# Performance work log

Measured on AMD Instinct MI355X. Metric: run time of the kernel, lower is better.

Reference implementation:

```python
import jax, jax.numpy as jnp
import numpy as np

N_GRAPHS = 64   # number of graphs in the batch
H = 128         # hidden dim
L = 3           # num_conv_layers
OUT = 64        # out_feature


def setup_inputs() -> dict:
    key = jax.random.key(0)
    ks = jax.random.split(key, 12)
    N, E, R, C = 10000, 160000, 2, 2
    s = 1.0 / np.sqrt(H)
    inp = {
        'x': jax.random.normal(ks[0], (N, H), jnp.float32),
        'edge_attr': jax.random.normal(ks[1], (E, H), jnp.float32),
        'node_mask': jax.random.uniform(ks[2], (R, C, N, 1), jnp.float32),
        'bond_W': jax.random.normal(ks[3], (L, H, H), jnp.float32) * s,
        'bond_b': jnp.zeros((L, H), jnp.float32),
        'eps': jnp.zeros((L,), jnp.float32),
        'conv_W1': jax.random.normal(ks[4], (L, H, H), jnp.float32) * s,
        'conv_b1': jnp.zeros((L, H), jnp.float32),
        'conv_W2': jax.random.normal(ks[5], (L, H, H), jnp.float32) * s,
        'conv_b2': jnp.zeros((L, H), jnp.float32),
        'mlp_W1': jax.random.normal(ks[6], (H, H), jnp.float32) * s,
        'mlp_b1': jnp.zeros((H,), jnp.float32),
        'mlp_W2': jax.random.normal(ks[7], (H, OUT), jnp.float32) * s,
        'mlp_b2': jnp.zeros((OUT,), jnp.float32),
        'edge_index': jax.random.randint(ks[8], (2, E), 0, N),
        'batch': jnp.sort(jax.random.randint(ks[9], (N,), 0, N_GRAPHS)),
    }
    return inp


def reference(x, edge_attr, node_mask, bond_W, bond_b, eps,
              conv_W1, conv_b1, conv_W2, conv_b2,
              mlp_W1, mlp_b1, mlp_W2, mlp_b2,
              edge_index, batch):
    gelu = lambda v: jax.nn.gelu(v, approximate=False)  # torch exact gelu
    R, C, N, _ = node_mask.shape
    src, dst = edge_index[0], edge_index[1]
    # edge_mask[r,c,e] = node_mask[r,c,src[e]] * node_mask[r,c,dst[e]]
    edge_mask = node_mask[:, :, src, :] * node_mask[:, :, dst, :]  # [R,C,E,1]
    # replica-offset graph ids: [R*C*N]
    batch_full = jnp.tile(batch, R * C) + jnp.repeat(jnp.arange(R * C), N) * N_GRAPHS
    # x repeated over (R, C): [R,C,N,H]
    h = jnp.broadcast_to(x[None, None], (R, C, N, x.shape[-1]))
    for i in range(L):
        emb = edge_attr @ bond_W[i] + bond_b[i]                    # [E,H]
        msg = gelu(h[:, :, src, :] + emb[None, None]) * edge_mask  # [R,C,E,H]
        agg = jnp.zeros_like(h).at[:, :, dst, :].add(msg)          # scatter_sum
        out = (1.0 + eps[i]) * h + agg
        out = gelu(out @ conv_W1[i] + conv_b1[i]) @ conv_W2[i] + conv_b2[i]
        h = gelu(out)  # norm=Identity, dropout=0
    hf = h.reshape(-1, h.shape[-1])                               # [R*C*N,H]
    y = gelu(hf @ mlp_W1 + mlp_b1) @ mlp_W2 + mlp_b2              # [R*C*N,OUT]
    fm = node_mask.reshape(-1, 1)
    D = R * N_GRAPHS * C
    num = jax.ops.segment_sum(y * fm, batch_full, num_segments=D)
    den = jax.ops.segment_sum(fm, batch_full, num_segments=D)
    return num / jnp.maximum(den, 1e-12)
```

## Files before the change

### kernel.cpp

```cpp
#include <hip/hip_runtime.h>

constexpr int H    = 128;
constexpr int NN   = 10000;
constexpr int EE   = 160000;
constexpr int RCN  = 4;
constexpr int NG   = 64;
constexpr int OUTF = 64;
constexpr int DSEG = 256;

using short8 = __attribute__((ext_vector_type(8))) short;
using f32x4  = __attribute__((ext_vector_type(4))) float;

__device__ __forceinline__ float gelu_f(float x){
  float z  = x*0.70710678118654752440f;
  float az = fabsf(z);
  float t  = __builtin_amdgcn_rcpf(fmaf(az, 0.3275911f, 1.0f));
  float e  = __expf(-z*z);
  float poly = fmaf(fmaf(fmaf(fmaf(1.061405429f, t, -1.453152027f),
                              t, 1.421413741f),
                         t, -0.284496736f),
                    t, 0.254829592f) * t;
  float er = fmaf(-poly, e, 1.0f);
  er = copysignf(er, z);
  return 0.5f*x*(1.0f + er);
}

__device__ __forceinline__ void split2(float x, unsigned short& h, unsigned short& m){
  unsigned int u = __float_as_uint(x);
  unsigned int rh = u + 0x7FFF + ((u>>16)&1);
  h = (unsigned short)(rh>>16);
  float fh = __uint_as_float((unsigned int)h << 16);
  float r1 = x - fh;
  unsigned int u1 = __float_as_uint(r1);
  unsigned int rm = u1 + 0x7FFF + ((u1>>16)&1);
  m = (unsigned short)(rm>>16);
}

__device__ __forceinline__ unsigned short bf16rne(float x){
  unsigned int u = __float_as_uint(x);
  return (unsigned short)((u + 0x7FFF + ((u>>16)&1))>>16);
}
__device__ __forceinline__ float bf2f(unsigned short v){
  return __uint_as_float((unsigned int)v << 16);
}

__global__ void k_hist(const int* __restrict__ dst, int* __restrict__ cnt){
  int e = blockIdx.x*256 + threadIdx.x;
  if(e < EE) atomicAdd(&cnt[dst[e]], 1);
}

__global__ __launch_bounds__(1024) void k_scan(const int* __restrict__ cnt,
                                               int* __restrict__ rs, int* __restrict__ cur){
  __shared__ int part[1024];
  int t = threadIdx.x;
  const int CH = 10;
  int base = t*CH;
  int s = 0;
  #pragma unroll
  for(int j=0;j<CH;j++){ int i = base+j; if(i<NN) s += cnt[i]; }
  part[t] = s;
  __syncthreads();
  for(int off=1; off<1024; off<<=1){
    int v = (t>=off) ? part[t-off] : 0;
    __syncthreads();
    part[t] += v;
    __syncthreads();
  }
  int run = (t==0) ? 0 : part[t-1];
  #pragma unroll
  for(int j=0;j<CH;j++){
    int i = base+j;
    if(i<NN){ rs[i] = run; cur[i] = run; run += cnt[i]; }
  }
  if(t == 1023) rs[NN] = part[1023];
}

__global__ void k_fill(const int* __restrict__ dst,
                       int* __restrict__ cur, int* __restrict__ eid){
  int e = blockIdx.x*256 + threadIdx.x;
  if(e >= EE) return;
  int p = atomicAdd(&cur[dst[e]], 1);
  eid[p] = e;
}

__global__ __launch_bounds__(256) void k_sortcsr(const int* __restrict__ rs, int* __restrict__ eid,
                          const int* __restrict__ src, int* __restrict__ esrc){
  int wid  = (blockIdx.x*256 + threadIdx.x) >> 6;
  int lane = threadIdx.x & 63;
  if(wid >= NN) return;
  int jb = rs[wid], je = rs[wid+1];
  int deg = je - jb;
  if(deg <= 0) return;
  if(deg == 1){
    if(lane == 0) esrc[jb] = src[eid[jb]];
    return;
  }
  if(deg <= 64){
    int v = (lane < deg) ? eid[jb + lane] : 0x7FFFFFFF;
    #pragma unroll
    for(int k=2; k<=64; k<<=1){
      #pragma unroll
      for(int j=k>>1; j>0; j>>=1){
        int o = __shfl_xor(v, j, 64);
        bool desc  = (lane & k) != 0;
        bool lower = (lane & j) == 0;
        v = ((lower != desc) ? min(v,o) : max(v,o));
      }
    }
    if(lane < deg){
      eid[jb+lane]  = v;
      esrc[jb+lane] = src[v];
    }
  } else if(lane == 0){
    for(int j=jb+1; j<je; j++){
      int v = eid[j];
      int k = j-1;
      while(k >= jb && eid[k] > v){ eid[k+1] = eid[k]; k--; }
      eid[k+1] = v;
    }
    for(int j=jb; j<je; j++) esrc[j] = src[eid[j]];
  }
}

__global__ void k_gbounds(const int* __restrict__ batch, int* __restrict__ gs){
  int g = threadIdx.x;
  if(g > NG) return;
  if(g == NG){ gs[NG] = NN; return; }
  int lo = 0, hi = NN;
  while(lo < hi){
    int mid = (lo+hi)>>1;
    if(batch[mid] < g) lo = mid+1; else hi = mid;
  }
  gs[g] = lo;
}

__global__ void k_emaskp(const int* __restrict__ src, const int* __restrict__ dst,
                         const int* __restrict__ eid, const float* __restrict__ nm,
                         float4* __restrict__ em4p){
  int j = blockIdx.x*256 + threadIdx.x;
  if(j >= EE) return;
  int e = eid[j];
  int s = src[e], d = dst[e];
  float4 m;
  m.x = nm[0*NN+s]*nm[0*NN+d];
  m.y = nm[1*NN+s]*nm[1*NN+d];
  m.z = nm[2*NN+s]*nm[2*NN+d];
  m.w = nm[3*NN+s]*nm[3*NN+d];
  em4p[j] = m;
}

__global__ void k_splitW(const float* __restrict__ W, unsigned short* __restrict__ oh,
                         unsigned short* __restrict__ om, int nmat, int N){
  int tid = blockIdx.x*256 + threadIdx.x;
  int total = nmat*128*N;
  if(tid >= total) return;
  int mat = tid / (128*N);
  int rem = tid - mat*(128*N);
  int k = rem / N;
  int n = rem - k*N;
  int NF = N >> 4;
  int ks = k >> 5, kk = k & 31;
  int nf = n >> 4;
  int lane = (n & 15) + 16*((kk & 15) >> 2);
  int e = 4*(kk >> 4) + (kk & 3);
  size_t idx = (size_t)mat*128*N + ((size_t)(ks*NF + nf)*64 + lane)*8 + e;
  unsigned short hh, mm;
  split2(W[tid], hh, mm);
  oh[idx] = hh; om[idx] = mm;
}

__global__ void k_splitA(const float* __restrict__ A, const int* __restrict__ eid,
                         unsigned short* __restrict__ oh){
  int tid = blockIdx.x*256 + threadIdx.x;
  if(tid >= EE*32) return;
  int j = tid >> 5, kq = tid & 31;
  int k = kq*4;
  int rsrc = eid[j];
  float4 v = *(const float4*)&A[(size_t)rsrc*H + k];
  ushort4 hh;
  hh.x = bf16rne(v.x); hh.y = bf16rne(v.y);
  hh.z = bf16rne(v.z); hh.w = bf16rne(v.w);
  *(ushort4*)&oh[(size_t)j*H + k] = hh;
}

template<int NFO, bool A2, bool GELU, int OMODE>
__global__ __launch_bounds__(256) void k_sgemm(
    const unsigned short* __restrict__ Ah, const unsigned short* __restrict__ Am,
    const unsigned short* __restrict__ Wh, const unsigned short* __restrict__ Wm,
    const float* __restrict__ bias, float* __restrict__ Cf,
    unsigned short* __restrict__ Oh, unsigned short* __restrict__ Om, int nrows){
  int t = threadIdx.x;
  int w = t >> 6, lane = t & 63;
  int m15 = lane & 15, kg = lane >> 4;
  int rowbase = blockIdx.x*128;

  const int SMAX = 4*NFO - 1;
  auto ldW = [&](int s, short8* d){
    size_t widx = ((size_t)s*64 + lane)*8;
    d[0] = *(const short8*)&Wh[widx];
    d[1] = *(const short8*)&Wm[widx];
  };

  int arow[2];
  #pragma unroll
  for(int mf=0;mf<2;mf++){
    int r = rowbase + w*32 + mf*16 + m15;
    arow[mf] = (r < nrows) ? r : (nrows-1);
  }

  f32x4 acc[2][NFO];
  #pragma unroll
  for(int mf=0;mf<2;mf++)
    #pragma unroll
    for(int nf=0;nf<NFO;nf++) acc[mf][nf] = (f32x4){0.f,0.f,0.f,0.f};

  short8 cw[2], nw[2];
  ldW(0, cw);
  ldW(1 <= SMAX ? 1 : SMAX, nw);

  for(int ks=0;ks<4;ks++){
    short8 ah[2], am[2];
    #pragma unroll
    for(int mf=0;mf<2;mf++){
      size_t base = (size_t)arow[mf]*H + ks*32 + kg*4;
      ushort4 hlo = *(const ushort4*)&Ah[base];
      ushort4 hhi = *(const ushort4*)&Ah[base + 16];
      ah[mf] = (short8){(short)hlo.x,(short)hlo.y,(short)hlo.z,(short)hlo.w,
                        (short)hhi.x,(short)hhi.y,(short)hhi.z,(short)hhi.w};
      if(A2){
        ushort4 mlo = *(const ushort4*)&Am[base];
        ushort4 mhi = *(const ushort4*)&Am[base + 16];
        am[mf] = (short8){(short)mlo.x,(short)mlo.y,(short)mlo.z,(short)mlo.w,
                          (short)mhi.x,(short)mhi.y,(short)mhi.z,(short)mhi.w};
      }
    }
    #pragma unroll
    for(int nf=0;nf<NFO;nf++){
      int s = ks*NFO + nf;
      short8 pw[2];
      ldW(s+2 <= SMAX ? s+2 : SMAX, pw);
      #pragma unroll
      for(int mf=0;mf<2;mf++){
        acc[mf][nf] = __builtin_amdgcn_mfma_f32_16x16x32_bf16(ah[mf], cw[0], acc[mf][nf], 0,0,0);
        acc[mf][nf] = __builtin_amdgcn_mfma_f32_16x16x32_bf16(ah[mf], cw[1], acc[mf][nf], 0,0,0);
        if(A2)
          acc[mf][nf] = __builtin_amdgcn_mfma_f32_16x16x32_bf16(am[mf], cw[0], acc[mf][nf], 0,0,0);
      }
      cw[0]=nw[0]; cw[1]=nw[1];
      nw[0]=pw[0]; nw[1]=pw[1];
    }
  }
  #pragma unroll
  for(int mf=0;mf<2;mf++){
    #pragma unroll
    for(int nf=0;nf<NFO;nf++){
      int gcol = nf*16 + m15;
      float bv = bias[gcol];
      #pragma unroll
      for(int r=0;r<4;r++){
        int grow = rowbase + w*32 + mf*16 + kg*4 + r;
        if(grow >= nrows) continue;
        float v = acc[mf][nf][r] + bv;
        if(GELU) v = gelu_f(v);
        size_t idx = (size_t)grow*(NFO*16) + gcol;
        if(OMODE == 0) Cf[idx] = v;
        if(OMODE == 1){
          unsigned short hh, mm2;
          split2(v, hh, mm2);
          Oh[idx] = hh; Om[idx] = mm2;
        }
        if(OMODE == 2) Oh[idx] = bf16rne(v);
      }
    }
  }
}

template<bool FIRST>
__global__ __launch_bounds__(256) void k_agg(const float* __restrict__ hin,
                       const unsigned short* __restrict__ embB, const float4* __restrict__ em4p,
                       const int* __restrict__ rs, const int* __restrict__ esrc,
                       const float* __restrict__ epsp,
                       unsigned short* __restrict__ Th, unsigned short* __restrict__ Tm){
  int t = threadIdx.x;
  int w = t >> 6;
  int lane = t & 63;
  int half = lane >> 5;
  int l32 = lane & 31;
  int n = blockIdx.x*4 + w;
  int d0 = l32*4;
  int rc0 = half*2, rc1 = rc0+1;
  float4 acc0 = {0.f,0.f,0.f,0.f}, acc1 = {0.f,0.f,0.f,0.f};
  int jb = rs[n], je = rs[n+1];

  float4 evs[3], h0s[3], h1s[3];
  float  m0s[3], m1s[3];

  auto ld = [&](int j, int slot){
    int s = esrc[j];
    ushort4 e4 = *(const ushort4*)&embB[(size_t)j*H + d0];
    evs[slot].x = bf2f(e4.x); evs[slot].y = bf2f(e4.y);
    evs[slot].z = bf2f(e4.z); evs[slot].w = bf2f(e4.w);
    float4 m = em4p[j];
    m0s[slot] = half ? m.z : m.x;
    m1s[slot] = half ? m.w : m.y;
    if(FIRST){
      h0s[slot] = *(const float4*)&hin[(size_t)s*H + d0];
      h1s[slot] = h0s[slot];
    } else {
      h0s[slot] = *(const float4*)&hin[((size_t)s*RCN + rc0)*H + d0];
      h1s[slot] = *(const float4*)&hin[((size_t)s*RCN + rc1)*H + d0];
    }
  };

  if(jb < je){
    ld(jb, 0);
    if(jb+1 < je) ld(jb+1, 1);
    if(jb+2 < je) ld(jb+2, 2);
    for(int j=jb; j<je; j++){
      float4 ev0 = evs[0], h00 = h0s[0], h10 = h1s[0];
      float  m00 = m0s[0], m10 = m1s[0];
      evs[0]=evs[1]; h0s[0]=h0s[1]; h1s[0]=h1s[1]; m0s[0]=m0s[1]; m1s[0]=m1s[1];
      evs[1]=evs[2]; h0s[1]=h0s[2]; h1s[1]=h1s[2]; m0s[1]=m0s[2]; m1s[1]=m1s[2];
      if(j+3 < je) ld(j+3, 2);
      if(FIRST){
        float gx = gelu_f(h00.x+ev0.x);
        float gy = gelu_f(h00.y+ev0.y);
        float gz = gelu_f(h00.z+ev0.z);
        float gw = gelu_f(h00.w+ev0.w);
        acc0.x += gx*m00; acc0.y += gy*m00; acc0.z += gz*m00; acc0.w += gw*m00;
        acc1.x += gx*m10; acc1.y += gy*m10; acc1.z += gz*m10; acc1.w += gw*m10;
      } else {
        acc0.x += gelu_f(h00.x+ev0.x)*m00;
        acc0.y += gelu_f(h00.y+ev0.y)*m00;
        acc0.z += gelu_f(h00.z+ev0.z)*m00;
        acc0.w += gelu_f(h00.w+ev0.w)*m00;
        acc1.x += gelu_f(h10.x+ev0.x)*m10;
        acc1.y += gelu_f(h10.y+ev0.y)*m10;
        acc1.z += gelu_f(h10.z+ev0.z)*m10;
        acc1.w += gelu_f(h10.w+ev0.w)*m10;
      }
    }
  }
  float e1 = 1.0f + epsp[0];
  #pragma unroll
  for(int p=0;p<2;p++){
    int rc = p ? rc1 : rc0;
    float4 ac = p ? acc1 : acc0;
    const float* hb = FIRST ? (hin + (size_t)n*H) : (hin + ((size_t)n*RCN + rc)*H);
    float4 hv = *(const float4*)&hb[d0];
    float4 o;
    o.x = e1*hv.x + ac.x; o.y = e1*hv.y + ac.y;
    o.z = e1*hv.z + ac.z; o.w = e1*hv.w + ac.w;
    int row = n*RCN + rc;
    ushort4 hh, mm;
    split2(o.x, hh.x, mm.x);
    split2(o.y, hh.y, mm.y);
    split2(o.z, hh.z, mm.z);
    split2(o.w, hh.w, mm.w);
    size_t idx = (size_t)row*H + d0;
    *(ushort4*)&Th[idx] = hh;
    *(ushort4*)&Tm[idx] = mm;
  }
}

__global__ __launch_bounds__(64) void k_pool(const float* __restrict__ y, const float* __restrict__ nm,
                       const int* __restrict__ gs, float* __restrict__ out){
  int seg = blockIdx.x;
  int rc = seg / NG;
  int g  = seg - rc*NG;
  int c  = threadIdx.x;
  int nb = gs[g], ne = gs[g+1];
  float num = 0.f, den = 0.f;
  for(int n=nb; n<ne; n++){
    float w = nm[rc*NN + n];
    num += y[((size_t)n*RCN + rc)*OUTF + c] * w;
    den += w;
  }
  out[seg*OUTF + c] = num / fmaxf(den, 1e-12f);
}

extern "C" void kernel_launch(void* const* d_in, const int* in_sizes, int n_in,
                              void* d_out, int out_size, void* d_ws, size_t ws_size,
                              hipStream_t stream){
  const float* x         = (const float*)d_in[0];
  const float* edge_attr = (const float*)d_in[1];
  const float* node_mask = (const float*)d_in[2];
  const float* bond_W    = (const float*)d_in[3];
  const float* bond_b    = (const float*)d_in[4];
  const float* epsv      = (const float*)d_in[5];
  const float* conv_W1   = (const float*)d_in[6];
  const float* conv_b1   = (const float*)d_in[7];
  const float* conv_W2   = (const float*)d_in[8];
  const float* conv_b2   = (const float*)d_in[9];
  const float* mlp_W1    = (const float*)d_in[10];
  const float* mlp_b1    = (const float*)d_in[11];
  const float* mlp_W2    = (const float*)d_in[12];
  const float* mlp_b2    = (const float*)d_in[13];
  const int*   eidx      = (const int*)d_in[14];
  const int*   batch     = (const int*)d_in[15];
  const int* srcp = eidx;
  const int* dstp = eidx + EE;

  char* p = (char*)d_ws;
  auto alloc = [&](size_t bytes)->char*{
    char* r = p; p += (bytes + 255) & ~size_t(255); return r;
  };
  float*  h    = (float*) alloc((size_t)RCN*NN*H*4);
  unsigned short* embB = (unsigned short*)alloc((size_t)EE*H*2);
  float4* em4p = (float4*)alloc((size_t)EE*16);
  float*  y    = (float*) alloc((size_t)RCN*NN*OUTF*4);
  int*    cnt  = (int*)   alloc((size_t)NN*4);
  int*    rs   = (int*)   alloc((size_t)(NN+1)*4);
  int*    cur  = (int*)   alloc((size_t)NN*4);
  int*    eid  = (int*)   alloc((size_t)EE*4);
  int*    esrc = (int*)   alloc((size_t)EE*4);
  int*    gs   = (int*)   alloc((size_t)(NG+1)*4);
  unsigned short* WBh  = (unsigned short*)alloc((size_t)3*16384*2);
  unsigned short* WBm  = (unsigned short*)alloc((size_t)3*16384*2);
  unsigned short* WC1h = (unsigned short*)alloc((size_t)3*16384*2);
  unsigned short* WC1m = (unsigned short*)alloc((size_t)3*16384*2);
  unsigned short* WC2h = (unsigned short*)alloc((size_t)3*16384*2);
  unsigned short* WC2m = (unsigned short*)alloc((size_t)3*16384*2);
  unsigned short* WM1h = (unsigned short*)alloc((size_t)16384*2);
  unsigned short* WM1m = (unsigned short*)alloc((size_t)16384*2);
  unsigned short* WM2h = (unsigned short*)alloc((size_t)8192*2);
  unsigned short* WM2m = (unsigned short*)alloc((size_t)8192*2);
  unsigned short* EAh  = (unsigned short*)alloc((size_t)EE*H*2);
  const size_t NPB = (size_t)RCN*NN*H*2;
  unsigned short* TBh = (unsigned short*)alloc(NPB);
  unsigned short* TBm = (unsigned short*)alloc(NPB);
  unsigned short* Uh  = (unsigned short*)alloc(NPB);
  unsigned short* Um  = (unsigned short*)alloc(NPB);
  if((size_t)(p - (char*)d_ws) > ws_size) return;

  hipMemsetAsync(cnt, 0, (size_t)NN*4, stream);

  k_hist    <<<(EE+255)/256, 256, 0, stream>>>(dstp, cnt);
  k_scan    <<<1, 1024, 0, stream>>>(cnt, rs, cur);
  k_fill    <<<(EE+255)/256, 256, 0, stream>>>(dstp, cur, eid);
  k_sortcsr <<<(NN*64+255)/256, 256, 0, stream>>>(rs, eid, srcp, esrc);
  k_emaskp  <<<(EE+255)/256, 256, 0, stream>>>(srcp, dstp, eid, node_mask, em4p);
  k_splitA  <<<EE*32/256, 256, 0, stream>>>(edge_attr, eid, EAh);
  k_gbounds <<<1, 128, 0, stream>>>(batch, gs);
  k_splitW  <<<192, 256, 0, stream>>>(bond_W,  WBh,  WBm,  3, 128);
  k_splitW  <<<192, 256, 0, stream>>>(conv_W1, WC1h, WC1m, 3, 128);
  k_splitW  <<<192, 256, 0, stream>>>(conv_W2, WC2h, WC2m, 3, 128);
  k_splitW  <<<64,  256, 0, stream>>>(mlp_W1,  WM1h, WM1m, 1, 128);
  k_splitW  <<<32,  256, 0, stream>>>(mlp_W2,  WM2h, WM2m, 1, 64);

  const int NROWS = RCN*NN;
  const int GB_E = EE/128;
  const int GB_N = (NROWS+127)/128;
  for(int l=0; l<3; l++){
    size_t wo = (size_t)l*16384;
    k_sgemm<8,false,false,2><<<GB_E, 256, 0, stream>>>(
        EAh, nullptr, WBh+wo, WBm+wo, bond_b + l*H, nullptr, embB, nullptr, EE);
    if(l == 0)
      k_agg<true ><<<NN/4, 256, 0, stream>>>(x, embB, em4p, rs, esrc, epsv + l, TBh, TBm);
    else
      k_agg<false><<<NN/4, 256, 0, stream>>>(h, embB, em4p, rs, esrc, epsv + l, TBh, TBm);
    k_sgemm<8,true,true,1><<<GB_N, 256, 0, stream>>>(
        TBh, TBm, WC1h+wo, WC1m+wo, conv_b1 + l*H, nullptr, Uh, Um, NROWS);
    if(l < 2)
      k_sgemm<8,true,true,0><<<GB_N, 256, 0, stream>>>(
          Uh, Um, WC2h+wo, WC2m+wo, conv_b2 + l*H, h, nullptr, nullptr, NROWS);
    else
      k_sgemm<8,true,true,1><<<GB_N, 256, 0, stream>>>(
          Uh, Um, WC2h+wo, WC2m+wo, conv_b2 + l*H, nullptr, TBh, TBm, NROWS);
  }
  k_sgemm<8,true,true,1><<<GB_N, 256, 0, stream>>>(
      TBh, TBm, WM1h, WM1m, mlp_b1, nullptr, Uh, Um, NROWS);
  k_sgemm<4,true,false,0><<<GB_N, 256, 0, stream>>>(
      Uh, Um, WM2h, WM2m, mlp_b2, y, nullptr, nullptr, NROWS);
  k_pool<<<DSEG, 64, 0, stream>>>(y, node_mask, gs, (float*)d_out);
}
```

Measured before the change: 613.3 us.

## Fuse back-to-back GEMM pairs through LDS and rotate aggregation prefetch registers

Adds a k_fuse2 kernel that computes the first GEMM plus GELU, keeps the split bf16 hi/lo intermediate in shared memory per wave, and then runs the second GEMM from LDS. This replaces the two-kernel conv MLP and final MLP chains, removing the round trip of the intermediate U buffers through global memory and some launches. The aggregation loop is also reworked to rotate three named register slots instead of shifting arrays, avoiding register moves. In exchange, the 67KB LDS footprint per block limits occupancy. In the last layer the kernel also reads and writes TBh/TBm in place, which is only safe because each block reads its own rows before writing them.

```diff
diff --git a/kernel.cpp b/kernel.cpp
--- a/kernel.cpp
+++ b/kernel.cpp
@@ -275,6 +275,201 @@
   }
 }
 
+template<int NFO2, bool G2, int OMODE>
+__global__ __launch_bounds__(256) void k_fuse2(
+    const unsigned short* __restrict__ Ah, const unsigned short* __restrict__ Am,
+    const unsigned short* __restrict__ W1h, const unsigned short* __restrict__ W1m,
+    const float* __restrict__ b1,
+    const unsigned short* __restrict__ W2h, const unsigned short* __restrict__ W2m,
+    const float* __restrict__ b2,
+    float* __restrict__ Cf,
+    unsigned short* __restrict__ Oh, unsigned short* __restrict__ Om, int nrows){
+  __shared__ unsigned int Ul[4*32*132];
+  int t = threadIdx.x;
+  int w = t >> 6, lane = t & 63;
+  int m15 = lane & 15, kg = lane >> 4;
+  int rowbase = blockIdx.x*128;
+  unsigned int* Uw = &Ul[w*32*132];
+
+  int arow[2];
+  #pragma unroll
+  for(int mf=0;mf<2;mf++){
+    int r = rowbase + w*32 + mf*16 + m15;
+    arow[mf] = (r < nrows) ? r : (nrows-1);
+  }
+
+  {
+    const int SMAX = 31;
+    auto ldW = [&](int s, short8* d){
+      size_t widx = ((size_t)s*64 + lane)*8;
+      d[0] = *(const short8*)&W1h[widx];
+      d[1] = *(const short8*)&W1m[widx];
+    };
+    f32x4 acc[2][8];
+    #pragma unroll
+    for(int mf=0;mf<2;mf++)
+      #pragma unroll
+      for(int nf=0;nf<8;nf++) acc[mf][nf] = (f32x4){0.f,0.f,0.f,0.f};
+    short8 cw[2], nw[2];
+    ldW(0, cw); ldW(1, nw);
+    for(int ks=0;ks<4;ks++){
+      short8 ah[2], am[2];
+      #pragma unroll
+      for(int mf=0;mf<2;mf++){
+        size_t base = (size_t)arow[mf]*H + ks*32 + kg*4;
+        ushort4 hlo = *(const ushort4*)&Ah[base];
+        ushort4 hhi = *(const ushort4*)&Ah[base + 16];
+        ushort4 mlo = *(const ushort4*)&Am[base];
+        ushort4 mhi = *(const ushort4*)&Am[base + 16];
+        ah[mf] = (short8){(short)hlo.x,(short)hlo.y,(short)hlo.z,(short)hlo.w,
+                          (short)hhi.x,(short)hhi.y,(short)hhi.z,(short)hhi.w};
+        am[mf] = (short8){(short)mlo.x,(short)mlo.y,(short)mlo.z,(short)mlo.w,
+                          (short)mhi.x,(short)mhi.y,(short)mhi.z,(short)mhi.w};
+      }
+      #pragma unroll
+      for(int nf=0;nf<8;nf++){
+        int s = ks*8 + nf;
+        short8 pw[2];
+        ldW(s+2 <= SMAX ? s+2 : SMAX, pw);
+        #pragma unroll
+        for(int mf=0;mf<2;mf++){
+          acc[mf][nf] = __builtin_amdgcn_mfma_f32_16x16x32_bf16(ah[mf], cw[0], acc[mf][nf], 0,0,0);
+          acc[mf][nf] = __builtin_amdgcn_mfma_f32_16x16x32_bf16(ah[mf], cw[1], acc[mf][nf], 0,0,0);
+          acc[mf][nf] = __builtin_amdgcn_mfma_f32_16x16x32_bf16(am[mf], cw[0], acc[mf][nf], 0,0,0);
+        }
+        cw[0]=nw[0]; cw[1]=nw[1];
+        nw[0]=pw[0]; nw[1]=pw[1];
+      }
+    }
+    #pragma unroll
+    for(int mf=0;mf<2;mf++){
+      #pragma unroll
+      for(int nf=0;nf<8;nf++){
+        float bv = b1[nf*16 + m15];
+        #pragma unroll
+        for(int r=0;r<4;r++){
+          float v = gelu_f(acc[mf][nf][r] + bv);
+          unsigned short hh, mm2;
+          split2(v, hh, mm2);
+          int wrow = mf*16 + kg*4 + r;
+          Uw[wrow*132 + nf*16 + m15] = (unsigned)hh | ((unsigned)mm2 << 16);
+        }
+      }
+    }
+  }
+  __syncthreads();
+
+  {
+    const int SMAX = 4*NFO2 - 1;
+    auto ldW = [&](int s, short8* d){
+      size_t widx = ((size_t)s*64 + lane)*8;
+      d[0] = *(const short8*)&W2h[widx];
+      d[1] = *(const short8*)&W2m[widx];
+    };
+    f32x4 acc[2][NFO2];
+    #pragma unroll
+    for(int mf=0;mf<2;mf++)
+      #pragma unroll
+      for(int nf=0;nf<NFO2;nf++) acc[mf][nf] = (f32x4){0.f,0.f,0.f,0.f};
+    short8 cw[2], nw[2];
+    ldW(0, cw); ldW(1 <= SMAX ? 1 : SMAX, nw);
+    for(int ks=0;ks<4;ks++){
+      short8 ah[2], am[2];
+      #pragma unroll
+      for(int mf=0;mf<2;mf++){
+        const unsigned int* base = &Uw[(mf*16 + m15)*132 + ks*32 + kg*4];
+        uint4 q0 = *(const uint4*)base;
+        uint4 q1 = *(const uint4*)(base + 16);
+        unsigned h0 = (q0.x & 0xFFFFu) | (q0.y << 16);
+        unsigned h1 = (q0.z & 0xFFFFu) | (q0.w << 16);
+        unsigned h2 = (q1.x & 0xFFFFu) | (q1.y << 16);
+        unsigned h3 = (q1.z & 0xFFFFu) | (q1.w << 16);
+        unsigned M0 = (q0.x >> 16) | (q0.y & 0xFFFF0000u);
+        unsigned M1 = (q0.z >> 16) | (q0.w & 0xFFFF0000u);
+        unsigned M2 = (q1.x >> 16) | (q1.y & 0xFFFF0000u);
+        unsigned M3 = (q1.z >> 16) | (q1.w & 0xFFFF0000u);
+        union { uint4 u; short8 s; } cvh, cvm;
+        cvh.u = (uint4){h0,h1,h2,h3};
+        cvm.u = (uint4){M0,M1,M2,M3};
+        ah[mf] = cvh.s; am[mf] = cvm.s;
+      }
+      #pragma unroll
+      for(int nf=0;nf<NFO2;nf++){
+        int s = ks*NFO2 + nf;
+        short8 pw[2];
+        ldW(s+2 <= SMAX ? s+2 : SMAX, pw);
+        #pragma unroll
+        for(int mf=0;mf<2;mf++){
+          acc[mf][nf] = __builtin_amdgcn_mfma_f32_16x16x32_bf16(ah[mf], cw[0], acc[mf][nf], 0,0,0);
+          acc[mf][nf] = __builtin_amdgcn_mfma_f32_16x16x32_bf16(ah[mf], cw[1], acc[mf][nf], 0,0,0);
+          acc[mf][nf] = __builtin_amdgcn_mfma_f32_16x16x32_bf16(am[mf], cw[0], acc[mf][nf], 0,0,0);
+        }
+        cw[0]=nw[0]; cw[1]=nw[1];
+        nw[0]=pw[0]; nw[1]=pw[1];
+      }
+    }
+    #pragma unroll
+    for(int mf=0;mf<2;mf++){
+      #pragma unroll
+      for(int nf=0;nf<NFO2;nf++){
+        int gcol = nf*16 + m15;
+        float bv = b2[gcol];
+        #pragma unroll
+        for(int r=0;r<4;r++){
+          int grow = rowbase + w*32 + mf*16 + kg*4 + r;
+          if(grow >= nrows) continue;
+          float v = acc[mf][nf][r] + bv;
+          if(G2) v = gelu_f(v);
+          size_t idx = (size_t)grow*(NFO2*16) + gcol;
+          if(OMODE == 0) Cf[idx] = v;
+          if(OMODE == 1){
+            unsigned short hh, mm2;
+            split2(v, hh, mm2);
+            Oh[idx] = hh; Om[idx] = mm2;
+          }
+        }
+      }
+    }
+  }
+}
+
+#define AGG_LD(J, EV, H0, H1, M0, M1) do{                                   \
+    int s_ = esrc[(J)];                                                     \
+    ushort4 e4_ = *(const ushort4*)&embB[(size_t)(J)*H + d0];               \
+    EV.x = bf2f(e4_.x); EV.y = bf2f(e4_.y);                                 \
+    EV.z = bf2f(e4_.z); EV.w = bf2f(e4_.w);                                 \
+    float4 m_ = em4p[(J)];                                                  \
+    M0 = half ? m_.z : m_.x;                                                \
+    M1 = half ? m_.w : m_.y;                                                \
+    if(FIRST){                                                              \
+      H0 = *(const float4*)&hin[(size_t)s_*H + d0];                         \
+      H1 = H0;                                                              \
+    } else {                                                                \
+      H0 = *(const float4*)&hin[((size_t)s_*RCN + rc0)*H + d0];             \
+      H1 = *(const float4*)&hin[((size_t)s_*RCN + rc1)*H + d0];             \
+    }                                                                       \
+  }while(0)
+
+#define AGG_STEP(EV, H0, H1, M0, M1) do{                                    \
+    if(FIRST){                                                              \
+      float gx = gelu_f(H0.x+EV.x);                                         \
+      float gy = gelu_f(H0.y+EV.y);                                         \
+      float gz = gelu_f(H0.z+EV.z);                                         \
+      float gw = gelu_f(H0.w+EV.w);                                         \
+      acc0.x += gx*M0; acc0.y += gy*M0; acc0.z += gz*M0; acc0.w += gw*M0;   \
+      acc1.x += gx*M1; acc1.y += gy*M1; acc1.z += gz*M1; acc1.w += gw*M1;   \
+    } else {                                                                \
+      acc0.x += gelu_f(H0.x+EV.x)*M0;                                       \
+      acc0.y += gelu_f(H0.y+EV.y)*M0;                                       \
+      acc0.z += gelu_f(H0.z+EV.z)*M0;                                       \
+      acc0.w += gelu_f(H0.w+EV.w)*M0;                                       \
+      acc1.x += gelu_f(H1.x+EV.x)*M1;                                       \
+      acc1.y += gelu_f(H1.y+EV.y)*M1;                                       \
+      acc1.z += gelu_f(H1.z+EV.z)*M1;                                       \
+      acc1.w += gelu_f(H1.w+EV.w)*M1;                                       \
+    }                                                                       \
+  }while(0)
+
 template<bool FIRST>
 __global__ __launch_bounds__(256) void k_agg(const float* __restrict__ hin,
                        const unsigned short* __restrict__ embB, const float4* __restrict__ em4p,
@@ -292,53 +487,24 @@
   float4 acc0 = {0.f,0.f,0.f,0.f}, acc1 = {0.f,0.f,0.f,0.f};
   int jb = rs[n], je = rs[n+1];
 
-  float4 evs[3], h0s[3], h1s[3];
-  float  m0s[3], m1s[3];
-
-  auto ld = [&](int j, int slot){
-    int s = esrc[j];
-    ushort4 e4 = *(const ushort4*)&embB[(size_t)j*H + d0];
-    evs[slot].x = bf2f(e4.x); evs[slot].y = bf2f(e4.y);
-    evs[slot].z = bf2f(e4.z); evs[slot].w = bf2f(e4.w);
-    float4 m = em4p[j];
-    m0s[slot] = half ? m.z : m.x;
-    m1s[slot] = half ? m.w : m.y;
-    if(FIRST){
-      h0s[slot] = *(const float4*)&hin[(size_t)s*H + d0];
-      h1s[slot] = h0s[slot];
-    } else {
-      h0s[slot] = *(const float4*)&hin[((size_t)s*RCN + rc0)*H + d0];
-      h1s[slot] = *(const float4*)&hin[((size_t)s*RCN + rc1)*H + d0];
-    }
-  };
+  float4 ev0, h00, h10, ev1, h01, h11, ev2, h02, h12;
+  float  m00, m10, m01, m11, m02, m12;
 
   if(jb < je){
-    ld(jb, 0);
-    if(jb+1 < je) ld(jb+1, 1);
-    if(jb+2 < je) ld(jb+2, 2);
-    for(int j=jb; j<je; j++){
-      float4 ev0 = evs[0], h00 = h0s[0], h10 = h1s[0];
-      float  m00 = m0s[0], m10 = m1s[0];
-      evs[0]=evs[1]; h0s[0]=h0s[1]; h1s[0]=h1s[1]; m0s[0]=m0s[1]; m1s[0]=m1s[1];
-      evs[1]=evs[2]; h0s[1]=h0s[2]; h1s[1]=h1s[2]; m0s[1]=m0s[2]; m1s[1]=m1s[2];
-      if(j+3 < je) ld(j+3, 2);
-      if(FIRST){
-        float gx = gelu_f(h00.x+ev0.x);
-        float gy = gelu_f(h00.y+ev0.y);
-        float gz = gelu_f(h00.z+ev0.z);
-        float gw = gelu_f(h00.w+ev0.w);
-        acc0.x += gx*m00; acc0.y += gy*m00; acc0.z += gz*m00; acc0.w += gw*m00;
-        acc1.x += gx*m10; acc1.y += gy*m10; acc1.z += gz*m10; acc1.w += gw*m10;
-      } else {
-        acc0.x += gelu_f(h00.x+ev0.x)*m00;
-        acc0.y += gelu_f(h00.y+ev0.y)*m00;
-        acc0.z += gelu_f(h00.z+ev0.z)*m00;
-        acc0.w += gelu_f(h00.w+ev0.w)*m00;
-        acc1.x += gelu_f(h10.x+ev0.x)*m10;
-        acc1.y += gelu_f(h10.y+ev0.y)*m10;
-        acc1.z += gelu_f(h10.z+ev0.z)*m10;
-        acc1.w += gelu_f(h10.w+ev0.w)*m10;
-      }
+    AGG_LD(jb, ev0, h00, h10, m00, m10);
+    if(jb+1 < je) AGG_LD(jb+1, ev1, h01, h11, m01, m11);
+    if(jb+2 < je) AGG_LD(jb+2, ev2, h02, h12, m02, m12);
+    int j = jb;
+    for(;;){
+      AGG_STEP(ev0, h00, h10, m00, m10);
+      if(j+3 < je) AGG_LD(j+3, ev0, h00, h10, m00, m10);
+      if(++j >= je) break;
+      AGG_STEP(ev1, h01, h11, m01, m11);
+      if(j+3 < je) AGG_LD(j+3, ev1, h01, h11, m01, m11);
+      if(++j >= je) break;
+      AGG_STEP(ev2, h02, h12, m02, m12);
+      if(j+3 < je) AGG_LD(j+3, ev2, h02, h12, m02, m12);
+      if(++j >= je) break;
     }
   }
   float e1 = 1.0f + epsp[0];
@@ -429,8 +595,6 @@
   const size_t NPB = (size_t)RCN*NN*H*2;
   unsigned short* TBh = (unsigned short*)alloc(NPB);
   unsigned short* TBm = (unsigned short*)alloc(NPB);
-  unsigned short* Uh  = (unsigned short*)alloc(NPB);
-  unsigned short* Um  = (unsigned short*)alloc(NPB);
   if((size_t)(p - (char*)d_ws) > ws_size) return;
 
   hipMemsetAsync(cnt, 0, (size_t)NN*4, stream);
@@ -459,18 +623,17 @@
       k_agg<true ><<<NN/4, 256, 0, stream>>>(x, embB, em4p, rs, esrc, epsv + l, TBh, TBm);
     else
       k_agg<false><<<NN/4, 256, 0, stream>>>(h, embB, em4p, rs, esrc, epsv + l, TBh, TBm);
-    k_sgemm<8,true,true,1><<<GB_N, 256, 0, stream>>>(
-        TBh, TBm, WC1h+wo, WC1m+wo, conv_b1 + l*H, nullptr, Uh, Um, NROWS);
     if(l < 2)
-      k_sgemm<8,true,true,0><<<GB_N, 256, 0, stream>>>(
-          Uh, Um, WC2h+wo, WC2m+wo, conv_b2 + l*H, h, nullptr, nullptr, NROWS);
+      k_fuse2<8,true,0><<<GB_N, 256, 0, stream>>>(
+          TBh, TBm, WC1h+wo, WC1m+wo, conv_b1 + l*H,
+          WC2h+wo, WC2m+wo, conv_b2 + l*H, h, nullptr, nullptr, NROWS);
     else
-      k_sgemm<8,true,true,1><<<GB_N, 256, 0, stream>>>(
-          Uh, Um, WC2h+wo, WC2m+wo, conv_b2 + l*H, nullptr, TBh, TBm, NROWS);
-  }
-  k_sgemm<8,true,true,1><<<GB_N, 256, 0, stream>>>(
-      TBh, TBm, WM1h, WM1m, mlp_b1, nullptr, Uh, Um, NROWS);
-  k_sgemm<4,true,false,0><<<GB_N, 256, 0, stream>>>(
-      Uh, Um, WM2h, WM2m, mlp_b2, y, nullptr, nullptr, NROWS);
+      k_fuse2<8,true,1><<<GB_N, 256, 0, stream>>>(
+          TBh, TBm, WC1h+wo, WC1m+wo, conv_b1 + l*H,
+          WC2h+wo, WC2m+wo, conv_b2 + l*H, nullptr, TBh, TBm, NROWS);
+  }
+  k_fuse2<4,false,0><<<GB_N, 256, 0, stream>>>(
+      TBh, TBm, WM1h, WM1m, mlp_b1, WM2h, WM2m, mlp_b2,
+      y, nullptr, nullptr, NROWS);
   k_pool<<<DSEG, 64, 0, stream>>>(y, node_mask, gs, (float*)d_out);
 }
```

Measured after the change: 559.0 us. 8.9% less time.
